# Kernel optimization log

Measured on AMD Instinct MI355X. Metric: run time of the kernel, lower is better.

Reference implementation:

```python
import jax, jax.numpy as jnp
import numpy as np

INPUT_SIZE, HIDDEN_SIZE, OUTPUT_SIZE = 2, 512, 512
ALPHA = 0.1


def setup_inputs() -> dict:
    key = jax.random.key(0)
    ks = jax.random.split(key, 8)
    B, T = 256, 512
    inputs = jax.random.normal(ks[0], (B, T, INPUT_SIZE), dtype=jnp.float32)
    init_context = jax.random.normal(ks[1], (B, OUTPUT_SIZE), dtype=jnp.float32)
    # parameters (torch Linear convention: y = x @ W.T + b)
    W_in = jax.random.normal(ks[2], (HIDDEN_SIZE, INPUT_SIZE), dtype=jnp.float32) * (1.0 / np.sqrt(INPUT_SIZE + HIDDEN_SIZE))
    b_in = jnp.zeros((HIDDEN_SIZE,), dtype=jnp.float32)
    # orthogonal-ish recurrent weight via QR
    A = jax.random.normal(ks[3], (HIDDEN_SIZE, HIDDEN_SIZE), dtype=jnp.float32)
    W_rec, _ = jnp.linalg.qr(A)
    W_rec = W_rec.astype(jnp.float32)
    b_rec = jnp.zeros((HIDDEN_SIZE,), dtype=jnp.float32)
    W_out = jax.random.normal(ks[4], (OUTPUT_SIZE, HIDDEN_SIZE), dtype=jnp.float32) * (1.0 / np.sqrt(HIDDEN_SIZE + OUTPUT_SIZE))
    W_h_init = jax.random.normal(ks[5], (HIDDEN_SIZE, OUTPUT_SIZE), dtype=jnp.float32) * (1.0 / np.sqrt(HIDDEN_SIZE + OUTPUT_SIZE))
    return {"inputs": inputs, "init_context": init_context, "W_in": W_in, "b_in": b_in,
            "W_rec": W_rec, "b_rec": b_rec, "W_out": W_out, "W_h_init": W_h_init}


def reference(inputs, init_context, W_in, b_in, W_rec, b_rec, W_out, W_h_init):
    # inputs: (B, T, I); init_context: (B, O)
    h0 = init_context @ W_h_init.T  # (B, H)
    # precompute input projection for all timesteps: (B, T, H)
    x_proj = jnp.einsum('bti,hi->bth', inputs, W_in) + b_in

    def step(h, x_t):
        h_new = (1.0 - ALPHA) * h + ALPHA * jnp.tanh(x_t + h @ W_rec.T + b_rec)
        return h_new, h_new

    # scan over time: move T to leading axis
    _, hs = jax.lax.scan(step, h0, jnp.swapaxes(x_proj, 0, 1))  # hs: (T, B, H)
    hidden_states = jnp.swapaxes(hs, 0, 1)  # (B, T, H)
    outputs = jnp.einsum('bth,oh->bto', hidden_states, W_out)  # (B, T, O)
    return hidden_states, outputs
```

## Files before the change

### kernel.cpp

```cpp
#include <hip/hip_runtime.h>

typedef __bf16 bf16x8 __attribute__((ext_vector_type(8)));
typedef float f32x4 __attribute__((ext_vector_type(4)));
typedef unsigned int u32x4 __attribute__((ext_vector_type(4)));

union UQ { uint4 q; u32x4 p; bf16x8 v; __bf16 b[8]; unsigned long long d[2]; };

__device__ __forceinline__ unsigned short f2bf(float x){
  union { float f; unsigned u; } c; c.f = x;
  return (unsigned short)((c.u + 0x7fffu + ((c.u >> 16) & 1u)) >> 16);
}

__global__ void zero_flags(int* __restrict__ p){
  p[threadIdx.x] = 0;
}

__global__ void pack_kernel(const float* __restrict__ W, uint4* __restrict__ dst){
  int tid  = blockIdx.x * 512 + threadIdx.x;
  int lane = tid & 63;
  int kt   = (tid >> 6) & 15;
  int ntl  = tid >> 10;
  int row  = ntl * 16 + (lane & 15);
  int k0   = kt * 32 + ((lane >> 4) << 3);
  const float* s = &W[row * 512 + k0];
  unsigned a0 = f2bf(s[0]) | ((unsigned)f2bf(s[1]) << 16);
  unsigned a1 = f2bf(s[2]) | ((unsigned)f2bf(s[3]) << 16);
  unsigned a2 = f2bf(s[4]) | ((unsigned)f2bf(s[5]) << 16);
  unsigned a3 = f2bf(s[6]) | ((unsigned)f2bf(s[7]) << 16);
  dst[tid] = (uint4){a0, a1, a2, a3};
}

__global__ void h0_kernel(const float* __restrict__ init, const float* __restrict__ Whi,
                          float* __restrict__ h0, unsigned short* __restrict__ hb0){
  int b = blockIdx.x, n = threadIdx.x;
  __shared__ float ic[512];
  ic[n] = init[b * 512 + n];
  __syncthreads();
  const float4* wr = (const float4*)&Whi[n * 512];
  float s = 0.f;
  #pragma unroll 8
  for (int o = 0; o < 128; o++){
    float4 w = wr[o];
    s += w.x * ic[4*o] + w.y * ic[4*o+1] + w.z * ic[4*o+2] + w.w * ic[4*o+3];
  }
  h0[b * 512 + n] = s;
  hb0[b * 512 + n] = f2bf(s);
}

__global__ __launch_bounds__(512, 1)
void rnn_gemm(const float* __restrict__ inputs, const float* __restrict__ W_in,
              const float* __restrict__ b_in, const float* __restrict__ b_rec,
              const uint4* __restrict__ wfrag, const uint4* __restrict__ wofrag,
              const float* __restrict__ h0, const unsigned short* __restrict__ hb0,
              int* __restrict__ progress, float* __restrict__ hidden,
              float* __restrict__ outp){
  __shared__ char smem[147456];
  const int bid = blockIdx.x;
  const int tid = threadIdx.x, w = tid >> 6, lane = tid & 63;
  const int col = lane & 15, quad = lane >> 4;

  if (bid < 16){
    const int m = bid;
    const int g16 = m << 4;
    const int nbase = w << 6;
    const int swc = (col & 7) << 3;
    unsigned short* hbuf = (unsigned short*)smem;
    uint4* wlds = (uint4*)(smem + 16384);

    UQ u[32];
    #pragma unroll
    for (int kt = 0; kt < 8; kt++)
      #pragma unroll
      for (int nt = 0; nt < 4; nt++){
        const uint4* src = &wfrag[(((w << 2) + nt) * 16 + kt) * 64 + lane];
        asm volatile("global_load_dwordx4 %0, %1, off"
                     : "=v"(u[kt * 4 + nt].p) : "v"(src) : "memory");
      }
    asm volatile("s_waitcnt vmcnt(0)" ::: "memory");
    #pragma unroll
    for (int j = 0; j < 32; j++)
      asm volatile("" : "+v"(u[j].d[0]), "+v"(u[j].d[1]));

    #pragma unroll
    for (int kt = 8; kt < 12; kt++)
      #pragma unroll
      for (int nt = 0; nt < 4; nt++)
        wlds[(w * 16 + (kt - 8) * 4 + nt) * 64 + lane] =
            wfrag[(((w << 2) + nt) * 16 + kt) * 64 + lane];

    UQ uaug[4];
    #pragma unroll
    for (int nt = 0; nt < 4; nt++){
      uaug[nt].d[0] = 0; uaug[nt].d[1] = 0;
      if (quad == 0){
        int n = nbase + nt * 16 + col;
        uaug[nt].b[0] = (__bf16)W_in[2 * n];
        uaug[nt].b[1] = (__bf16)W_in[2 * n + 1];
        uaug[nt].b[2] = (__bf16)(b_in[n] + b_rec[n]);
      }
    }

    float h[16];
    #pragma unroll
    for (int nt = 0; nt < 4; nt++){
      float4 h4 = *(const float4*)&h0[(g16 + col) * 512 + nbase + nt * 16 + (quad << 2)];
      h[nt*4+0] = h4.x; h[nt*4+1] = h4.y; h[nt*4+2] = h4.z; h[nt*4+3] = h4.w;
    }

    {
      int b = tid >> 5, n0 = (tid & 31) << 4;
      const uint4* s4 = (const uint4*)&hb0[(g16 + b) * 512 + n0];
      uint4 v0 = s4[0], v1 = s4[1];
      int sw = (b & 7) << 3;
      *(uint4*)&hbuf[(b << 9) + (n0 ^ sw)]       = v0;
      *(uint4*)&hbuf[(b << 9) + ((n0 + 8) ^ sw)] = v1;
    }
    __syncthreads();

    unsigned long long wsp = (unsigned long long)wfrag;
    const float2* xsrc = (const float2*)&inputs[((size_t)(g16 + col)) << 10];

#define ISSUE(b1) { const int kt_ = 12 + (b1);                                    \
    _Pragma("unroll")                                                             \
    for (int nt_ = 0; nt_ < 4; nt_++)                                             \
      sv[(b1)*4 + nt_].q = ws[(((w << 2) + nt_) * 16 + kt_) * 64 + lane]; }

#define HREAD(kt_) *(const uint4*)&hbuf[(col << 9) + ((((kt_) << 5) + (quad << 3)) ^ swc)]

    for (int t = 0; t < 512; t++){
      asm volatile("" : "+s"(wsp));
      const uint4* ws = (const uint4*)wsp;

      UQ baug; baug.d[0] = 0; baug.d[1] = 0;
      float2 xv = xsrc[t];
      if (quad == 0){
        baug.b[0] = (__bf16)xv.x; baug.b[1] = (__bf16)xv.y; baug.b[2] = (__bf16)1.0f;
      }

      f32x4 acc[4];
      #pragma unroll
      for (int nt = 0; nt < 4; nt++)
        acc[nt] = __builtin_amdgcn_mfma_f32_16x16x32_bf16(uaug[nt].v, baug.v,
                                                          (f32x4){0.f,0.f,0.f,0.f}, 0, 0, 0);

      UQ sv[16];
      ISSUE(0);
      UQ bh[16];
      #pragma unroll
      for (int kt = 0; kt < 16; kt++)
        bh[kt].q = HREAD(kt);

      #pragma unroll
      for (int kt = 0; kt < 8; kt++){
        #pragma unroll
        for (int nt = 0; nt < 4; nt++)
          acc[nt] = __builtin_amdgcn_mfma_f32_16x16x32_bf16(u[kt*4+nt].v, bh[kt].v, acc[nt], 0, 0, 0);
        if (kt == 0) ISSUE(1);
        if (kt == 2) ISSUE(2);
        if (kt == 4) ISSUE(3);
      }
      #pragma unroll
      for (int kt = 8; kt < 12; kt++){
        #pragma unroll
        for (int nt = 0; nt < 4; nt++){
          UQ a; a.q = wlds[(w * 16 + (kt - 8) * 4 + nt) * 64 + lane];
          acc[nt] = __builtin_amdgcn_mfma_f32_16x16x32_bf16(a.v, bh[kt].v, acc[nt], 0, 0, 0);
        }
      }
      #pragma unroll
      for (int kt = 12; kt < 16; kt++){
        #pragma unroll
        for (int nt = 0; nt < 4; nt++)
          acc[nt] = __builtin_amdgcn_mfma_f32_16x16x32_bf16(sv[(kt-12)*4+nt].v, bh[kt].v, acc[nt], 0, 0, 0);
      }

      __syncthreads();

      #pragma unroll
      for (int nt = 0; nt < 4; nt++){
        UQ hw; hw.d[0] = 0; hw.d[1] = 0;
        #pragma unroll
        for (int r = 0; r < 4; r++){
          float z  = acc[nt][r];
          float e  = __expf(2.0f * z);
          float rc = __builtin_amdgcn_rcpf(e + 1.0f);
          float hn = fmaf(0.9f, h[nt*4+r], 0.1f) - 0.2f * rc;
          h[nt*4+r] = hn;
          hw.b[r] = (__bf16)hn;
        }
        *(unsigned long long*)&hbuf[(col << 9) + ((nbase + (nt << 4) + (quad << 2)) ^ swc)] = hw.d[0];
        *(float4*)&hidden[((size_t)(g16 + col) * 512 + t) * 512 + nbase + (nt << 4) + (quad << 2)] =
            (float4){h[nt*4+0], h[nt*4+1], h[nt*4+2], h[nt*4+3]};
      }
      __syncthreads();

      if (((t + 1) & 63) == 0){
        asm volatile("s_waitcnt vmcnt(0)" ::: "memory");
        __syncthreads();
        if (tid == 0){
          __builtin_amdgcn_fence(__ATOMIC_RELEASE, "agent");
          __hip_atomic_store(&progress[m], t + 1, __ATOMIC_RELAXED, __HIP_MEMORY_SCOPE_AGENT);
        }
      }
    }
#undef ISSUE
#undef HREAD
  } else {
    const int gid = bid - 16;
    const int m0  = gid << 7;
    const int grp = gid >> 6;
    const int thr = (m0 & 511) + 128;
    const int ms  = w >> 1;
    const int nh  = w & 1;
    unsigned short* albf = (unsigned short*)smem;
    uint4* wq = (uint4*)(smem + 8192);

    if (tid == 0)
      while (__hip_atomic_load(&progress[grp], __ATOMIC_RELAXED,
                               __HIP_MEMORY_SCOPE_AGENT) < thr) {}
    __syncthreads();

    f32x4 acc[2][16];
    #pragma unroll
    for (int mt = 0; mt < 2; mt++)
      #pragma unroll
      for (int nt = 0; nt < 16; nt++) acc[mt][nt] = (f32x4){0.f, 0.f, 0.f, 0.f};

    for (int kt = 0; kt < 16; kt++){
      #pragma unroll
      for (int i = 0; i < 2; i++){
        int r  = (tid >> 3) + (i << 6);
        int c4 = (tid & 7) << 2;
        const unsigned long long* hp =
            (const unsigned long long*)&hidden[(size_t)(m0 + r) * 512 + (kt << 5) + c4];
        unsigned long long d0 = __hip_atomic_load(hp,     __ATOMIC_RELAXED, __HIP_MEMORY_SCOPE_AGENT);
        unsigned long long d1 = __hip_atomic_load(hp + 1, __ATOMIC_RELAXED, __HIP_MEMORY_SCOPE_AGENT);
        union { unsigned long long d[2]; float f[4]; } cv; cv.d[0] = d0; cv.d[1] = d1;
        unsigned lo = f2bf(cv.f[0]) | ((unsigned)f2bf(cv.f[1]) << 16);
        unsigned hi = f2bf(cv.f[2]) | ((unsigned)f2bf(cv.f[3]) << 16);
        int byteoff = (r << 6) + ((c4 << 1) ^ (((r >> 1) & 3) << 4));
        *(uint2*)(smem + byteoff) = (uint2){lo, hi};
      }
      #pragma unroll
      for (int j = 0; j < 4; j++){
        int idx = (j << 9) + tid;
        wq[(idx >> 6) * 64 + (idx & 63)] = wofrag[(((idx >> 6) << 4) + kt) * 64 + (idx & 63)];
      }
      __syncthreads();

      bf16x8 af[2];
      #pragma unroll
      for (int mt = 0; mt < 2; mt++){
        int rl = (ms << 5) + (mt << 4) + col;
        int byteoff = (rl << 6) + ((quad << 4) ^ (((rl >> 1) & 3) << 4));
        af[mt] = *(const bf16x8*)((const char*)albf + byteoff);
      }

      #pragma unroll
      for (int nt = 0; nt < 16; nt++){
        UQ uu; uu.q = wq[((nh << 4) + nt) * 64 + lane];
        acc[0][nt] = __builtin_amdgcn_mfma_f32_16x16x32_bf16(af[0], uu.v, acc[0][nt], 0, 0, 0);
        acc[1][nt] = __builtin_amdgcn_mfma_f32_16x16x32_bf16(af[1], uu.v, acc[1][nt], 0, 0, 0);
      }
      __syncthreads();
    }

    #pragma unroll
    for (int mt = 0; mt < 2; mt++)
      #pragma unroll
      for (int nt = 0; nt < 16; nt++)
        #pragma unroll
        for (int r = 0; r < 4; r++)
          outp[(size_t)(m0 + (ms << 5) + (mt << 4) + (quad << 2) + r) * 512
               + (nh << 8) + (nt << 4) + col] = acc[mt][nt][r];
  }
}

extern "C" void kernel_launch(void* const* d_in, const int* in_sizes, int n_in,
                              void* d_out, int out_size, void* d_ws, size_t ws_size,
                              hipStream_t stream){
  const float* inputs  = (const float*)d_in[0];
  const float* initc   = (const float*)d_in[1];
  const float* W_in    = (const float*)d_in[2];
  const float* b_in    = (const float*)d_in[3];
  const float* W_rec   = (const float*)d_in[4];
  const float* b_rec   = (const float*)d_in[5];
  const float* W_out   = (const float*)d_in[6];
  const float* W_hi    = (const float*)d_in[7];

  float* hidden  = (float*)d_out;
  float* outputs = hidden + (size_t)67108864;

  char* ws = (char*)d_ws;
  uint4*          wrec_f  = (uint4*)ws;
  uint4*          wout_f  = (uint4*)(ws + (512 << 10));
  float*          h0      = (float*)(ws + (1024 << 10));
  unsigned short* hb0     = (unsigned short*)(ws + (1536 << 10));
  int*            progress= (int*)(ws + (1792 << 10));

  zero_flags<<<1, 64, 0, stream>>>(progress);
  pack_kernel<<<64, 512, 0, stream>>>(W_rec, wrec_f);
  pack_kernel<<<64, 512, 0, stream>>>(W_out, wout_f);
  h0_kernel<<<256, 512, 0, stream>>>(initc, W_hi, h0, hb0);
  rnn_gemm<<<1040, 512, 0, stream>>>(inputs, W_in, b_in, b_rec, wrec_f, wout_f,
                                     h0, hb0, progress, hidden, outputs);
}
```

Before: 1.804 ms.

## Retile output GEMM blocks to 64 rows per batch-time chunk with full-K staging

The output-projection blocks now each cover 64 timesteps of one batch element (64 rows) instead of 128 rows, so the grid grows from 1040 to 2064 blocks. Each block waits on its own batch group's progress for its time chunk. Its entire 64x512 hidden tile is loaded and converted to bf16 in LDS once, up front, rather than per k-step. The aim is to let the output GEMM start earlier and overlap more with the recurrence, and to cut per-iteration global loads. In exchange it uses more LDS per block (64KB plus the weight buffer) and does half the MFMA work per weight fragment load, which lowers weight reuse.

```diff
diff --git a/kernel.cpp b/kernel.cpp
--- a/kernel.cpp
+++ b/kernel.cpp
@@ -207,40 +207,51 @@
 #undef HREAD
   } else {
     const int gid = bid - 16;
-    const int m0  = gid << 7;
-    const int grp = gid >> 6;
-    const int thr = (m0 & 511) + 128;
+    const int tchunk = gid >> 8;
+    const int b   = gid & 255;
+    const int t0  = tchunk << 6;
+    const int m0  = (b << 9) + t0;
+    const int grp = b >> 4;
     const int ms  = w >> 1;
     const int nh  = w & 1;
     unsigned short* albf = (unsigned short*)smem;
-    uint4* wq = (uint4*)(smem + 8192);
+    uint4* wq = (uint4*)(smem + 65536);
 
     if (tid == 0)
       while (__hip_atomic_load(&progress[grp], __ATOMIC_RELAXED,
-                               __HIP_MEMORY_SCOPE_AGENT) < thr) {}
+                               __HIP_MEMORY_SCOPE_AGENT) < t0 + 64) {}
     __syncthreads();
 
-    f32x4 acc[2][16];
-    #pragma unroll
-    for (int mt = 0; mt < 2; mt++)
-      #pragma unroll
-      for (int nt = 0; nt < 16; nt++) acc[mt][nt] = (f32x4){0.f, 0.f, 0.f, 0.f};
+    {
+      const int r  = tid >> 3;
+      const int c0 = (tid & 7) << 6;
+      const unsigned long long* hp =
+          (const unsigned long long*)&hidden[(size_t)(m0 + r) * 512 + c0];
+      unsigned long long dv[32];
+      #pragma unroll
+      for (int j = 0; j < 32; j++)
+        dv[j] = __hip_atomic_load(hp + j, __ATOMIC_RELAXED, __HIP_MEMORY_SCOPE_AGENT);
+      const int sw = (r & 7) << 4;
+      #pragma unroll
+      for (int g = 0; g < 8; g++){
+        union { unsigned long long d[4]; float f[8]; } cv;
+        cv.d[0] = dv[g*4]; cv.d[1] = dv[g*4+1]; cv.d[2] = dv[g*4+2]; cv.d[3] = dv[g*4+3];
+        uint4 o;
+        o.x = f2bf(cv.f[0]) | ((unsigned)f2bf(cv.f[1]) << 16);
+        o.y = f2bf(cv.f[2]) | ((unsigned)f2bf(cv.f[3]) << 16);
+        o.z = f2bf(cv.f[4]) | ((unsigned)f2bf(cv.f[5]) << 16);
+        o.w = f2bf(cv.f[6]) | ((unsigned)f2bf(cv.f[7]) << 16);
+        int byteoff = (r << 10) + ((((c0 + (g << 3)) << 1)) ^ sw);
+        *(uint4*)((char*)albf + byteoff) = o;
+      }
+    }
+    __syncthreads();
+
+    f32x4 acc[16];
+    #pragma unroll
+    for (int nt = 0; nt < 16; nt++) acc[nt] = (f32x4){0.f, 0.f, 0.f, 0.f};
 
     for (int kt = 0; kt < 16; kt++){
-      #pragma unroll
-      for (int i = 0; i < 2; i++){
-        int r  = (tid >> 3) + (i << 6);
-        int c4 = (tid & 7) << 2;
-        const unsigned long long* hp =
-            (const unsigned long long*)&hidden[(size_t)(m0 + r) * 512 + (kt << 5) + c4];
-        unsigned long long d0 = __hip_atomic_load(hp,     __ATOMIC_RELAXED, __HIP_MEMORY_SCOPE_AGENT);
-        unsigned long long d1 = __hip_atomic_load(hp + 1, __ATOMIC_RELAXED, __HIP_MEMORY_SCOPE_AGENT);
-        union { unsigned long long d[2]; float f[4]; } cv; cv.d[0] = d0; cv.d[1] = d1;
-        unsigned lo = f2bf(cv.f[0]) | ((unsigned)f2bf(cv.f[1]) << 16);
-        unsigned hi = f2bf(cv.f[2]) | ((unsigned)f2bf(cv.f[3]) << 16);
-        int byteoff = (r << 6) + ((c4 << 1) ^ (((r >> 1) & 3) << 4));
-        *(uint2*)(smem + byteoff) = (uint2){lo, hi};
-      }
       #pragma unroll
       for (int j = 0; j < 4; j++){
         int idx = (j << 9) + tid;
@@ -248,31 +259,27 @@
       }
       __syncthreads();
 
-      bf16x8 af[2];
-      #pragma unroll
-      for (int mt = 0; mt < 2; mt++){
-        int rl = (ms << 5) + (mt << 4) + col;
-        int byteoff = (rl << 6) + ((quad << 4) ^ (((rl >> 1) & 3) << 4));
-        af[mt] = *(const bf16x8*)((const char*)albf + byteoff);
+      bf16x8 af;
+      {
+        int rl = (ms << 4) + col;
+        int byteoff = (rl << 10) + (((kt << 6) + (quad << 4)) ^ ((rl & 7) << 4));
+        af = *(const bf16x8*)((const char*)albf + byteoff);
       }
 
       #pragma unroll
       for (int nt = 0; nt < 16; nt++){
         UQ uu; uu.q = wq[((nh << 4) + nt) * 64 + lane];
-        acc[0][nt] = __builtin_amdgcn_mfma_f32_16x16x32_bf16(af[0], uu.v, acc[0][nt], 0, 0, 0);
-        acc[1][nt] = __builtin_amdgcn_mfma_f32_16x16x32_bf16(af[1], uu.v, acc[1][nt], 0, 0, 0);
+        acc[nt] = __builtin_amdgcn_mfma_f32_16x16x32_bf16(af, uu.v, acc[nt], 0, 0, 0);
       }
       __syncthreads();
     }
 
     #pragma unroll
-    for (int mt = 0; mt < 2; mt++)
-      #pragma unroll
-      for (int nt = 0; nt < 16; nt++)
-        #pragma unroll
-        for (int r = 0; r < 4; r++)
-          outp[(size_t)(m0 + (ms << 5) + (mt << 4) + (quad << 2) + r) * 512
-               + (nh << 8) + (nt << 4) + col] = acc[mt][nt][r];
+    for (int nt = 0; nt < 16; nt++)
+      #pragma unroll
+      for (int r = 0; r < 4; r++)
+        outp[(size_t)(m0 + (ms << 4) + (quad << 2) + r) * 512
+             + (nh << 8) + (nt << 4) + col] = acc[nt][r];
   }
 }
 
@@ -302,6 +309,6 @@
   pack_kernel<<<64, 512, 0, stream>>>(W_rec, wrec_f);
   pack_kernel<<<64, 512, 0, stream>>>(W_out, wout_f);
   h0_kernel<<<256, 512, 0, stream>>>(initc, W_hi, h0, hb0);
-  rnn_gemm<<<1040, 512, 0, stream>>>(inputs, W_in, b_in, b_rec, wrec_f, wout_f,
+  rnn_gemm<<<2064, 512, 0, stream>>>(inputs, W_in, b_in, b_rec, wrec_f, wout_f,
                                      h0, hb0, progress, hidden, outputs);
 }
```

After: 1.719 ms. 1.05x faster.
